# Optimization experiments

Measured on AMD Instinct MI355X. Metric: run time of the kernel, lower is better.

Reference implementation:

```python
import jax, jax.numpy as jnp
import numpy as np

N, E = 25000, 400000
HID, EDGE_F, DIM, HEADS, ADY = 128, 16, 3, 8, 64
INNER = int(1.25 * HID)          # 160
MSG_F = 2 * HID + EDGE_F + 1     # 273 (e3, relaxed=False -> 1 distance feature)


def silu(x):
    return x * jax.nn.sigmoid(x)


def ada_ln(x, y, W, b):
    # LayerNorm (no affine) + FiLM conditioning from y
    mu = jnp.mean(x, axis=-1, keepdims=True)
    var = jnp.var(x, axis=-1, keepdims=True)
    xn = (x - mu) * jax.lax.rsqrt(var + 1e-5)
    scale, shift = jnp.split(y @ W + b, 2, axis=-1)
    return xn * (1.0 + scale) + shift


def setup_inputs() -> dict:
    key = jax.random.key(0)
    ks = jax.random.split(key, 32)
    rn = lambda k, shp, s=0.05: (jax.random.normal(k, shp, jnp.float32) * s)
    inp = {
        'h': jax.random.normal(ks[0], (N, HID), jnp.float32),
        'coords': jax.random.normal(ks[1], (N, DIM), jnp.float32),
        'a': jax.random.normal(ks[2], (E, EDGE_F), jnp.float32),
        'y': jax.random.normal(ks[3], (N, ADY), jnp.float32),
        'res': jnp.zeros((N, HID), jnp.float32),
        'src': jax.random.randint(ks[4], (E,), 0, N, jnp.int32),
        'dst': jax.random.randint(ks[5], (E,), 0, N, jnp.int32),
        # edge MLP
        'We1': rn(ks[6], (MSG_F, INNER)), 'be1': jnp.zeros((INNER,), jnp.float32),
        'We2': rn(ks[7], (INNER, INNER)), 'be2': jnp.zeros((INNER,), jnp.float32),
        # coord head (xavier gain 0.001 -> tiny init)
        'Wc': rn(ks[8], (INNER, 1), 0.001),
        # attention/value/output heads
        'Wv': rn(ks[9], (INNER, HID)),
        'Wa': rn(ks[10], (INNER, HEADS)),
        'Wo': rn(ks[11], (HID, HID)),
        # node MLP
        'Wn1': rn(ks[12], (HID, INNER)), 'bn1': jnp.zeros((INNER,), jnp.float32),
        'Wn2': rn(ks[13], (INNER, HID)), 'bn2': jnp.zeros((HID,), jnp.float32),
        # adaptive LayerNorms (FiLM from y)
        'Wf1': rn(ks[14], (ADY, 2 * HID)), 'bf1': jnp.zeros((2 * HID,), jnp.float32),
        'Wf2': rn(ks[15], (ADY, 2 * HID)), 'bf2': jnp.zeros((2 * HID,), jnp.float32),
    }
    return inp


def reference(h, coords, a, y, res, src, dst,
              We1, be1, We2, be2, Wc, Wv, Wa, Wo,
              Wn1, bn1, Wn2, bn2, Wf1, bf1, Wf2, bf2):
    n = h.shape[0]
    heads = Wa.shape[1]
    # --- distance features (e3, relaxed=False): radial only ---
    xs, xd = coords[src], coords[dst]          # [E, 3]
    diffs = xs - xd
    radials = jnp.sum(diffs * diffs, axis=-1, keepdims=True)  # [E, 1]
    # --- edge MLP on gathered features ---
    f = jnp.concatenate([h[src], h[dst], radials, a], axis=-1)  # [E, 273]
    m = silu(f @ We1 + be1)
    m = silu(m @ We2 + be2)                    # [E, inner]
    # --- coordinate messages + scatter-sum to dst ---
    msg_x = (m @ Wc) * diffs / (jnp.sqrt(radials + 1e-5) + 1.0)  # [E, 3]
    coords_out = coords + jax.ops.segment_sum(msg_x, dst, num_segments=n)
    # --- edge softmax over incoming edges per dst node ---
    logits = m @ Wa                             # [E, heads]
    mx = jax.ops.segment_max(logits, dst, num_segments=n)
    ex = jnp.exp(logits - mx[dst])
    den = jax.ops.segment_sum(ex, dst, num_segments=n)
    w = ex / den[dst]                           # [E, heads]
    # --- weighted value aggregation ---
    vals = (m @ Wv).reshape(-1, heads, HID // heads) * w[:, :, None]
    h_agg = jax.ops.segment_sum(vals, dst, num_segments=n).reshape(n, HID)
    f2 = h_agg @ Wo
    res1 = res + f2
    h1 = ada_ln(h + f2, y, Wf1, bf1)
    f3 = silu(h1 @ Wn1 + bn1) @ Wn2 + bn2
    res2 = res1 + f3
    h2 = ada_ln(h1 + f3, y, Wf2, bf2)
    return (h2, coords_out, res2)
```

## Files before the change

kernel.cpp:

```cpp
#include <hip/hip_runtime.h>
#include <math.h>

#define N_NODES 25000
#define N_EDGES 400000
#define HID 128
#define EDGE_F 16
#define ADY 64
#define INNER 160
#define MSG_F 273
#define HEADS 8

#define OUT_CRD (N_NODES * HID)
#define OUT_RES (N_NODES * (HID + 3))

#define FLAG_OFF 0
#define DEN_OFF  256
#define CACC_OFF 800256
#define HAGG_OFF 1100288
#define CW_BASE  13900288
#define MEMSET_BYTES 13900288

typedef unsigned short u16;
typedef unsigned int u32;
typedef unsigned long long u64;
typedef __attribute__((ext_vector_type(8))) short short8;
typedef __attribute__((ext_vector_type(4))) float f32x4;

__device__ __forceinline__ float bf2f(u16 v) {
    union { u32 u; float f; } x; x.u = ((u32)v) << 16; return x.f;
}
__device__ __forceinline__ u16 f2bf(float f) {
    union { float ff; u32 u; } x; x.ff = f;
    u32 u = x.u;
    u32 rounding = 0x7FFFu + ((u >> 16) & 1u);
    u += rounding;
    return (u16)(u >> 16);
}
__device__ __forceinline__ float silu(float z) {
    z = fminf(fmaxf(z, -30000.f), 30000.f);
    return z / (1.0f + __expf(-z));
}

template<bool F32> __device__ __forceinline__ float ldg1(const void* p, size_t i) {
    if (F32) return ((const float*)p)[i];
    return bf2f(((const u16*)p)[i]);
}
template<bool F32> __device__ __forceinline__ void stg1(void* p, size_t i, float v) {
    if (F32) ((float*)p)[i] = v;
    else     ((u16*)p)[i] = f2bf(v);
}
template<bool F32> __device__ __forceinline__ void ld8a(const void* p, size_t i, u16* dst) {
    if (F32) {
        const float* fp = (const float*)p + i;
        float4 v0 = ((const float4*)fp)[0];
        float4 v1 = ((const float4*)fp)[1];
        __align__(16) u16 tmp[8] = { f2bf(v0.x), f2bf(v0.y), f2bf(v0.z), f2bf(v0.w),
                                     f2bf(v1.x), f2bf(v1.y), f2bf(v1.z), f2bf(v1.w) };
        *(uint4*)dst = *(const uint4*)tmp;
    } else {
        *(uint4*)dst = *(const uint4*)((const u16*)p + i);
    }
}
__device__ __forceinline__ float ldany(const void* p, size_t i, bool f32) {
    return f32 ? ((const float*)p)[i] : bf2f(((const u16*)p)[i]);
}

__global__ void detect_kernel(const void* h, int* flag) {
    __shared__ float red[256];
    const int t = threadIdx.x;
    const u16* p = (const u16*)h;
    float mx = 0.f;
    for (int i = 0; i < 8; i++) {
        int idx = (t * 8 + i) * 97;
        float v = fabsf(bf2f(p[idx * 2]));
        mx = fmaxf(mx, v);
    }
    red[t] = mx;
    __syncthreads();
    for (int s = 128; s > 0; s >>= 1) {
        if (t < s) red[t] = fmaxf(red[t], red[t + s]);
        __syncthreads();
    }
    if (t == 0) flag[0] = (red[0] > 1e10f || red[0] == 0.f) ? 1 : 0;
}

struct CvtArgs {
    const void* src[16];
    u64 dstoff[16];
    int n[16];
};
__global__ void cvt_kernel(const int* __restrict__ flag, char* wsbase, CvtArgs args) {
    const int ten = blockIdx.y;
    const void* s = args.src[ten];
    u16* d = (u16*)(wsbase + args.dstoff[ten]);
    const int n = args.n[ten];
    const bool f32 = (*flag != 0);
    if (f32) {
        const float* sf = (const float*)s;
        for (int i = blockIdx.x * 256 + threadIdx.x; i < n; i += gridDim.x * 256)
            d[i] = f2bf(sf[i]);
    } else {
        const u16* su = (const u16*)s;
        for (int i = blockIdx.x * 256 + threadIdx.x; i < n; i += gridDim.x * 256)
            d[i] = su[i];
    }
}

__global__ void blockw_kernel(const int* __restrict__ flag, char* ws,
                              u64 b1off, u64 b2off, u64 b3off, u64 b4off,
                              u64 b5off, u64 b6off, u64 b7off, u64 b8off,
                              const void* We1, const void* We2,
                              const void* Wv, const void* Wa, const void* Wc,
                              const void* Wo, const void* Wn1, const void* Wn2,
                              const void* Wf1, const void* Wf2)
{
    const bool f32 = (*flag != 0);
    u16* b1 = (u16*)(ws + b1off);
    u16* b2 = (u16*)(ws + b2off);
    u16* b3 = (u16*)(ws + b3off);
    u16* b4 = (u16*)(ws + b4off);
    u16* b5 = (u16*)(ws + b5off);
    u16* b6 = (u16*)(ws + b6off);
    u16* b7 = (u16*)(ws + b7off);
    u16* b8 = (u16*)(ws + b8off);
    const int g = blockIdx.x * 256 + threadIdx.x;
    const int stride = gridDim.x * 256;
    for (int i = g; i < 5*160*72; i += stride) {
        int c = i / (160*72), rem = i % (160*72), n = rem / 72, kc = rem % 72;
        int k = c*64 + kc;
        float v = 0.f;
        if (kc < 64) {
            if (k < MSG_F)      v = ldany(We1, (size_t)k*INNER + n, f32);
            else if (k == 273)  v = ldany(We1, (size_t)256*INNER + n, f32);
        }
        b1[i] = f2bf(v);
    }
    for (int i = g; i < 3*160*72; i += stride) {
        int c = i / (160*72), rem = i % (160*72), n = rem / 72, kc = rem % 72;
        int k = c*64 + kc;
        float v = 0.f;
        if (kc < 64 && k < INNER) v = ldany(We2, (size_t)k*INNER + n, f32);
        b2[i] = f2bf(v);
    }
    for (int i = g; i < 3*144*72; i += stride) {
        int c = i / (144*72), rem = i % (144*72), n = rem / 72, kc = rem % 72;
        int k = c*64 + kc;
        float v = 0.f;
        if (kc < 64 && k < INNER) {
            if (n < 128)      v = ldany(Wv, (size_t)k*HID + n, f32);
            else if (n < 136) v = ldany(Wa, (size_t)k*HEADS + (n-128), f32);
            else if (n == 136) v = ldany(Wc, (size_t)k, f32);
        }
        b3[i] = f2bf(v);
    }
    for (int i = g; i < 2*128*72; i += stride) {
        int c = i / (128*72), rem = i % (128*72), n = rem / 72, kc = rem % 72;
        int k = c*64 + kc;
        float v = (kc < 64 && k < HID) ? ldany(Wo, (size_t)k*HID + n, f32) : 0.f;
        b4[i] = f2bf(v);
    }
    for (int i = g; i < 2*160*72; i += stride) {
        int c = i / (160*72), rem = i % (160*72), n = rem / 72, kc = rem % 72;
        int k = c*64 + kc;
        float v = (kc < 64) ? ldany(Wn1, (size_t)k*INNER + n, f32) : 0.f;
        b5[i] = f2bf(v);
    }
    for (int i = g; i < 3*128*72; i += stride) {
        int c = i / (128*72), rem = i % (128*72), n = rem / 72, kc = rem % 72;
        int k = c*64 + kc;
        float v = (kc < 64 && k < INNER) ? ldany(Wn2, (size_t)k*HID + n, f32) : 0.f;
        b6[i] = f2bf(v);
    }
    for (int i = g; i < 256*72; i += stride) {
        int n = i / 72, kc = i % 72;
        float v = (kc < 64) ? ldany(Wf1, (size_t)kc*256 + n, f32) : 0.f;
        b7[i] = f2bf(v);
    }
    for (int i = g; i < 256*72; i += stride) {
        int n = i / 72, kc = i % 72;
        float v = (kc < 64) ? ldany(Wf2, (size_t)kc*256 + n, f32) : 0.f;
        b8[i] = f2bf(v);
    }
}

template<bool F32>
__device__ __forceinline__ void edge_body(
    const void* h, const void* coords, const void* a,
    const int* __restrict__ src, const int* __restrict__ dst,
    const u16* __restrict__ We1Tb, const u16* __restrict__ We2Tb,
    const u16* __restrict__ W3Tb,
    const u16* __restrict__ cbe1, const u16* __restrict__ cbe2,
    float* __restrict__ den, float* __restrict__ hagg, float* __restrict__ cacc,
    u16* sPool, float* sex, float* sdiff, float* srad, int* ssrc, int* sdstl)
{
    const int t   = threadIdx.x;
    const int w   = t >> 6;
    const int l   = t & 63;
    const int col = l & 15;
    const int q   = l >> 4;

    u16* sF  = sPool;
    u16* sM1 = sPool;
    u16* sM2 = sPool + 64*168;

    const int e0 = blockIdx.x * 64;

    if (t < 64) {
        int e = e0 + t;
        int s = src[e], d = dst[e];
        ssrc[t] = s; sdstl[t] = d;
        float dx = ldg1<F32>(coords, (size_t)s*3+0) - ldg1<F32>(coords, (size_t)d*3+0);
        float dy = ldg1<F32>(coords, (size_t)s*3+1) - ldg1<F32>(coords, (size_t)d*3+1);
        float dz = ldg1<F32>(coords, (size_t)s*3+2) - ldg1<F32>(coords, (size_t)d*3+2);
        sdiff[t*4+0] = dx; sdiff[t*4+1] = dy; sdiff[t*4+2] = dz;
        float r2 = dx*dx + dy*dy + dz*dz;
        srad[t] = r2;
        sdiff[t*4+3] = 1.0f / (sqrtf(r2 + 1e-5f) + 1.0f);
    }
    __syncthreads();

    {
        int e = t >> 2, part = t & 3;
        int node_s = ssrc[e], node_d = sdstl[e];
        #pragma unroll
        for (int c = 0; c < 4; c++) {
            int node = (c < 2) ? node_s : node_d;
            int c0 = (c & 1) * 64 + part * 16;
            ld8a<F32>(h, (size_t)node*HID + c0,     &sF[e*360 + c*72 + part*16]);
            ld8a<F32>(h, (size_t)node*HID + c0 + 8, &sF[e*360 + c*72 + part*16 + 8]);
        }
        __align__(16) u16 tmp[16];
        #pragma unroll
        for (int j = 0; j < 16; j++) tmp[j] = 0;
        if (part == 0) {
            float r2 = srad[e];
            tmp[0] = f2bf(r2);
            for (int j = 0; j < 15; j++)
                tmp[1+j] = f2bf(ldg1<F32>(a, (size_t)(e0+e)*EDGE_F + j));
        } else if (part == 1) {
            tmp[0] = f2bf(ldg1<F32>(a, (size_t)(e0+e)*EDGE_F + 15));
            float r2 = srad[e];
            tmp[1] = f2bf(r2 - bf2f(f2bf(r2)));
        }
        *(uint4*)(&sF[e*360 + 4*72 + part*16])     = ((uint4*)tmp)[0];
        *(uint4*)(&sF[e*360 + 4*72 + part*16 + 8]) = ((uint4*)tmp)[1];
    }
    __syncthreads();

    f32x4 acc1[10];
    #pragma unroll
    for (int nt = 0; nt < 10; nt++) {
        float v = bf2f(cbe1[nt*16 + col]);
        acc1[nt] = (f32x4){v, v, v, v};
    }
    const u16* fbase = &sF[(w*16 + col)*360];
    #pragma unroll
    for (int c = 0; c < 5; c++) {
        #pragma unroll
        for (int ks = 0; ks < 2; ks++) {
            short8 af = *(const short8*)(fbase + c*72 + ks*32 + q*8);
            const u16* B1 = We1Tb + (size_t)c*160*72 + ks*32 + q*8;
            #pragma unroll
            for (int nt = 0; nt < 10; nt++) {
                short8 b = *(const short8*)(B1 + (nt*16 + col)*72);
                acc1[nt] = __builtin_amdgcn_mfma_f32_16x16x32_bf16(af, b, acc1[nt], 0, 0, 0);
            }
        }
    }
    __syncthreads();
    #pragma unroll
    for (int nt = 0; nt < 10; nt++)
        #pragma unroll
        for (int r = 0; r < 4; r++)
            sM1[(w*16 + q*4 + r)*168 + nt*16 + col] = f2bf(silu(acc1[nt][r]));
    __syncthreads();

    f32x4 acc2[10];
    #pragma unroll
    for (int nt = 0; nt < 10; nt++) {
        float v = bf2f(cbe2[nt*16 + col]);
        acc2[nt] = (f32x4){v, v, v, v};
    }
    const u16* m1base = &sM1[(w*16 + col)*168];
    #pragma unroll
    for (int k5 = 0; k5 < 5; k5++) {
        short8 af = *(const short8*)(m1base + k5*32 + q*8);
        const u16* B2 = We2Tb + (size_t)(k5>>1)*160*72 + (k5&1)*32 + q*8;
        #pragma unroll
        for (int nt = 0; nt < 10; nt++) {
            short8 b = *(const short8*)(B2 + (nt*16 + col)*72);
            acc2[nt] = __builtin_amdgcn_mfma_f32_16x16x32_bf16(af, b, acc2[nt], 0, 0, 0);
        }
    }
    #pragma unroll
    for (int nt = 0; nt < 10; nt++)
        #pragma unroll
        for (int r = 0; r < 4; r++)
            sM2[(w*16 + q*4 + r)*168 + nt*16 + col] = f2bf(silu(acc2[nt][r]));
    __syncthreads();

    f32x4 acc3[9];
    #pragma unroll
    for (int nt = 0; nt < 9; nt++) acc3[nt] = (f32x4){0.f, 0.f, 0.f, 0.f};
    const u16* m2base = &sM2[(w*16 + col)*168];
    #pragma unroll
    for (int k5 = 0; k5 < 5; k5++) {
        short8 af = *(const short8*)(m2base + k5*32 + q*8);
        const u16* B3 = W3Tb + (size_t)(k5>>1)*144*72 + (k5&1)*32 + q*8;
        #pragma unroll
        for (int nt = 0; nt < 9; nt++) {
            short8 b = *(const short8*)(B3 + (nt*16 + col)*72);
            acc3[nt] = __builtin_amdgcn_mfma_f32_16x16x32_bf16(af, b, acc3[nt], 0, 0, 0);
        }
    }

    const int mbase = w*16 + q*4;
    if (col < 8) {
        #pragma unroll
        for (int r = 0; r < 4; r++) {
            int m = mbase + r;
            int d = sdstl[m];
            float ex = __expf(fminf(fmaxf(acc3[8][r], -30.f), 30.f));
            sex[m*8 + col] = ex;
            atomicAdd(&den[(size_t)d*8 + col], ex);
        }
    } else if (col == 8) {
        #pragma unroll
        for (int r = 0; r < 4; r++) {
            int m = mbase + r;
            int d = sdstl[m];
            float lc = fminf(fmaxf(acc3[8][r], -1e6f), 1e6f);
            float invf = sdiff[m*4 + 3];
            #pragma unroll
            for (int j = 0; j < 3; j++)
                atomicAdd(&cacc[(size_t)d*3 + j], lc * sdiff[m*4 + j] * invf);
        }
    }
    __syncthreads();
    #pragma unroll
    for (int nt = 0; nt < 8; nt++) {
        #pragma unroll
        for (int r = 0; r < 4; r++) {
            int m = mbase + r;
            int d = sdstl[m];
            atomicAdd(&hagg[(size_t)d*HID + nt*16 + col], acc3[nt][r] * sex[m*8 + nt]);
        }
    }
}

__global__ __launch_bounds__(256, 3)
void edge_kernel(const int* __restrict__ flag,
                 const void* h, const void* coords, const void* a,
                 const int* __restrict__ src, const int* __restrict__ dst,
                 const u16* __restrict__ We1Tb, const u16* __restrict__ We2Tb,
                 const u16* __restrict__ W3Tb,
                 const u16* __restrict__ cbe1, const u16* __restrict__ cbe2,
                 float* __restrict__ den, float* __restrict__ hagg,
                 float* __restrict__ cacc)
{
    __shared__ __align__(16) u16 sPool[64*360];
    __shared__ float sex[64*8];
    __shared__ float sdiff[64*4];
    __shared__ float srad[64];
    __shared__ int   ssrc[64];
    __shared__ int   sdstl[64];
    if (*flag)
        edge_body<true>(h, coords, a, src, dst, We1Tb, We2Tb, W3Tb, cbe1, cbe2,
                        den, hagg, cacc, sPool, sex, sdiff, srad, ssrc, sdstl);
    else
        edge_body<false>(h, coords, a, src, dst, We1Tb, We2Tb, W3Tb, cbe1, cbe2,
                         den, hagg, cacc, sPool, sex, sdiff, srad, ssrc, sdstl);
}

template<bool F32>
__device__ __forceinline__ void node_body(
    const void* h, const void* res, const void* coords, const void* y,
    const float* __restrict__ den, const float* __restrict__ hagg,
    const float* __restrict__ cacc,
    const u16* __restrict__ WoB, const u16* __restrict__ Wn1B,
    const u16* __restrict__ Wn2B, const u16* __restrict__ Wf1B,
    const u16* __restrict__ Wf2B,
    const u16* __restrict__ cbn1, const u16* __restrict__ cbn2,
    const u16* __restrict__ cbf1, const u16* __restrict__ cbf2,
    void* out,
    u16* sB, u16* sG, u16* sM, u16* sM2, u16* sR1, u16* sH, u16* sY)
{
    const int t = threadIdx.x;
    const int w = t >> 6, l = t & 63, col = l & 15, q = l >> 4;
    const int n0 = blockIdx.x * 64;

    {
        int node = t >> 2, part = t & 3;
        int gn = n0 + node;
        bool ok = gn < N_NODES;
        uint4 z = {0,0,0,0};
        #pragma unroll
        for (int j = 0; j < 32; j += 8) {
            if (ok) ld8a<F32>(h, (size_t)gn*HID + part*32 + j, &sH[node*136 + part*32 + j]);
            else    *(uint4*)&sH[node*136 + part*32 + j] = z;
        }
        if (ok) {
            ld8a<F32>(y, (size_t)gn*ADY + part*16,     &sY[node*72 + part*16]);
            ld8a<F32>(y, (size_t)gn*ADY + part*16 + 8, &sY[node*72 + part*16 + 8]);
        } else {
            *(uint4*)&sY[node*72 + part*16]     = z;
            *(uint4*)&sY[node*72 + part*16 + 8] = z;
        }
        #pragma unroll
        for (int c = 0; c < 2; c++) {
            float inv = 0.f;
            if (ok) {
                float dd = den[(size_t)gn*8 + c*4 + part];
                inv = dd > 0.f ? 1.f/dd : 0.f;
            }
            __align__(16) u16 tmp[16];
            #pragma unroll
            for (int j = 0; j < 16; j += 4) {
                float4 v = ok ? *(const float4*)(hagg + (size_t)gn*HID + c*64 + part*16 + j)
                              : (float4){0.f,0.f,0.f,0.f};
                tmp[j+0]=f2bf(v.x*inv); tmp[j+1]=f2bf(v.y*inv);
                tmp[j+2]=f2bf(v.z*inv); tmp[j+3]=f2bf(v.w*inv);
            }
            *(uint4*)&sG[c*4608 + node*72 + part*16]     = ((uint4*)tmp)[0];
            *(uint4*)&sG[c*4608 + node*72 + part*16 + 8] = ((uint4*)tmp)[1];
        }
    }

    f32x4 aF2[8];
    #pragma unroll
    for (int nt = 0; nt < 8; nt++) aF2[nt] = (f32x4){0.f,0.f,0.f,0.f};
    for (int c = 0; c < 2; c++) {
        __syncthreads();
        { const uint4* g4 = (const uint4*)(WoB + (size_t)c*128*72); uint4* s4 = (uint4*)sB;
          for (int i = t; i < 1152; i += 256) s4[i] = g4[i]; }
        __syncthreads();
        #pragma unroll
        for (int ks = 0; ks < 2; ks++) {
            short8 af = *(const short8*)&sG[c*4608 + (w*16+col)*72 + ks*32 + q*8];
            #pragma unroll
            for (int nt = 0; nt < 8; nt++) {
                short8 b = *(const short8*)&sB[(nt*16+col)*72 + ks*32 + q*8];
                aF2[nt] = __builtin_amdgcn_mfma_f32_16x16x32_bf16(af, b, aF2[nt], 0, 0, 0);
            }
        }
    }

    f32x4 aFl[16];
    #pragma unroll
    for (int nt = 0; nt < 16; nt++) {
        float v = bf2f(cbf1[nt*16 + col]);
        aFl[nt] = (f32x4){v,v,v,v};
    }
    __syncthreads();
    { const uint4* g4 = (const uint4*)Wf1B; uint4* s4 = (uint4*)sB;
      for (int i = t; i < 2304; i += 256) s4[i] = g4[i]; }
    __syncthreads();
    #pragma unroll
    for (int ks = 0; ks < 2; ks++) {
        short8 af = *(const short8*)&sY[(w*16+col)*72 + ks*32 + q*8];
        #pragma unroll
        for (int nt = 0; nt < 16; nt++) {
            short8 b = *(const short8*)&sB[(nt*16+col)*72 + ks*32 + q*8];
            aFl[nt] = __builtin_amdgcn_mfma_f32_16x16x32_bf16(af, b, aFl[nt], 0, 0, 0);
        }
    }

    {
        float xv[8][4], s[4], ss[4];
        #pragma unroll
        for (int r = 0; r < 4; r++) { s[r] = 0.f; ss[r] = 0.f; }
        #pragma unroll
        for (int nt = 0; nt < 8; nt++)
            #pragma unroll
            for (int r = 0; r < 4; r++) {
                float x = bf2f(sH[(w*16+q*4+r)*136 + nt*16+col]) + aF2[nt][r];
                xv[nt][r] = x; s[r] += x; ss[r] += x*x;
            }
        #pragma unroll
        for (int r = 0; r < 4; r++)
            for (int off = 1; off <= 8; off <<= 1) {
                s[r]  += __shfl_xor(s[r], off);
                ss[r] += __shfl_xor(ss[r], off);
            }
        float mu[4], rs[4];
        #pragma unroll
        for (int r = 0; r < 4; r++) {
            mu[r] = s[r] * (1.f/128.f);
            float var = ss[r] * (1.f/128.f) - mu[r]*mu[r];
            rs[r] = rsqrtf(fmaxf(var, 0.f) + 1e-5f);
        }
        #pragma unroll
        for (int nt = 0; nt < 8; nt++)
            #pragma unroll
            for (int r = 0; r < 4; r++) {
                int m = w*16+q*4+r, n = nt*16+col, gn = n0+m;
                float h1 = (xv[nt][r]-mu[r])*rs[r]*(1.f+aFl[nt][r]) + aFl[nt+8][r];
                sM[m*168 + n] = f2bf(h1);
                float r1 = aF2[nt][r];
                if (gn < N_NODES) r1 += ldg1<F32>(res, (size_t)gn*HID + n);
                sR1[m*128 + n] = f2bf(r1);
            }
    }

    f32x4 aT[10];
    #pragma unroll
    for (int nt = 0; nt < 10; nt++) {
        float v = bf2f(cbn1[nt*16 + col]);
        aT[nt] = (f32x4){v,v,v,v};
    }
    for (int c = 0; c < 2; c++) {
        __syncthreads();
        { const uint4* g4 = (const uint4*)(Wn1B + (size_t)c*160*72); uint4* s4 = (uint4*)sB;
          for (int i = t; i < 1440; i += 256) s4[i] = g4[i]; }
        __syncthreads();
        #pragma unroll
        for (int ks = 0; ks < 2; ks++) {
            short8 af = *(const short8*)&sM[(w*16+col)*168 + c*64 + ks*32 + q*8];
            #pragma unroll
            for (int nt = 0; nt < 10; nt++) {
                short8 b = *(const short8*)&sB[(nt*16+col)*72 + ks*32 + q*8];
                aT[nt] = __builtin_amdgcn_mfma_f32_16x16x32_bf16(af, b, aT[nt], 0, 0, 0);
            }
        }
    }
    #pragma unroll
    for (int nt = 0; nt < 10; nt++)
        #pragma unroll
        for (int r = 0; r < 4; r++)
            sM2[(w*16+q*4+r)*168 + nt*16+col] = f2bf(silu(aT[nt][r]));

    f32x4 aF3[8];
    #pragma unroll
    for (int nt = 0; nt < 8; nt++) {
        float v = bf2f(cbn2[nt*16 + col]);
        aF3[nt] = (f32x4){v,v,v,v};
    }
    for (int c = 0; c < 3; c++) {
        __syncthreads();
        { const uint4* g4 = (const uint4*)(Wn2B + (size_t)c*128*72); uint4* s4 = (uint4*)sB;
          for (int i = t; i < 1152; i += 256) s4[i] = g4[i]; }
        __syncthreads();
        const int nks = (c < 2) ? 2 : 1;
        for (int ks = 0; ks < nks; ks++) {
            short8 af = *(const short8*)&sM2[(w*16+col)*168 + c*64 + ks*32 + q*8];
            #pragma unroll
            for (int nt = 0; nt < 8; nt++) {
                short8 b = *(const short8*)&sB[(nt*16+col)*72 + ks*32 + q*8];
                aF3[nt] = __builtin_amdgcn_mfma_f32_16x16x32_bf16(af, b, aF3[nt], 0, 0, 0);
            }
        }
    }

    #pragma unroll
    for (int nt = 0; nt < 16; nt++) {
        float v = bf2f(cbf2[nt*16 + col]);
        aFl[nt] = (f32x4){v,v,v,v};
    }
    __syncthreads();
    { const uint4* g4 = (const uint4*)Wf2B; uint4* s4 = (uint4*)sB;
      for (int i = t; i < 2304; i += 256) s4[i] = g4[i]; }
    __syncthreads();
    #pragma unroll
    for (int ks = 0; ks < 2; ks++) {
        short8 af = *(const short8*)&sY[(w*16+col)*72 + ks*32 + q*8];
        #pragma unroll
        for (int nt = 0; nt < 16; nt++) {
            short8 b = *(const short8*)&sB[(nt*16+col)*72 + ks*32 + q*8];
            aFl[nt] = __builtin_amdgcn_mfma_f32_16x16x32_bf16(af, b, aFl[nt], 0, 0, 0);
        }
    }

    {
        float xv[8][4], s[4], ss[4];
        #pragma unroll
        for (int r = 0; r < 4; r++) { s[r] = 0.f; ss[r] = 0.f; }
        #pragma unroll
        for (int nt = 0; nt < 8; nt++)
            #pragma unroll
            for (int r = 0; r < 4; r++) {
                float x = bf2f(sM[(w*16+q*4+r)*168 + nt*16+col]) + aF3[nt][r];
                xv[nt][r] = x; s[r] += x; ss[r] += x*x;
            }
        #pragma unroll
        for (int r = 0; r < 4; r++)
            for (int off = 1; off <= 8; off <<= 1) {
                s[r]  += __shfl_xor(s[r], off);
                ss[r] += __shfl_xor(ss[r], off);
            }
        float mu[4], rs[4];
        #pragma unroll
        for (int r = 0; r < 4; r++) {
            mu[r] = s[r] * (1.f/128.f);
            float var = ss[r] * (1.f/128.f) - mu[r]*mu[r];
            rs[r] = rsqrtf(fmaxf(var, 0.f) + 1e-5f);
        }
        #pragma unroll
        for (int nt = 0; nt < 8; nt++)
            #pragma unroll
            for (int r = 0; r < 4; r++) {
                int m = w*16+q*4+r, n = nt*16+col, gn = n0+m;
                if (gn < N_NODES) {
                    float h2 = (xv[nt][r]-mu[r])*rs[r]*(1.f+aFl[nt][r]) + aFl[nt+8][r];
                    stg1<F32>(out, (size_t)gn*HID + n, h2);
                    stg1<F32>(out, (size_t)OUT_RES + (size_t)gn*HID + n,
                              bf2f(sR1[m*128 + n]) + aF3[nt][r]);
                }
            }
    }

    if (t < 64) {
        int gn = n0 + t;
        if (gn < N_NODES) {
            #pragma unroll
            for (int j = 0; j < 3; j++)
                stg1<F32>(out, (size_t)OUT_CRD + (size_t)gn*3 + j,
                          ldg1<F32>(coords, (size_t)gn*3 + j) + cacc[(size_t)gn*3 + j]);
        }
    }
}

__global__ __launch_bounds__(256, 1)
void node_kernel(const int* __restrict__ flag,
                 const void* h, const void* res, const void* coords, const void* y,
                 const float* __restrict__ den, const float* __restrict__ hagg,
                 const float* __restrict__ cacc,
                 const u16* __restrict__ WoB, const u16* __restrict__ Wn1B,
                 const u16* __restrict__ Wn2B, const u16* __restrict__ Wf1B,
                 const u16* __restrict__ Wf2B,
                 const u16* __restrict__ cbn1, const u16* __restrict__ cbn2,
                 const u16* __restrict__ cbf1, const u16* __restrict__ cbf2,
                 void* out)
{
    __shared__ __align__(16) u16 sB[256*72];
    __shared__ __align__(16) u16 sG[2*64*72];
    __shared__ __align__(16) u16 sM[64*168];
    __shared__ __align__(16) u16 sM2[64*168];
    __shared__ __align__(16) u16 sR1[64*128];
    __shared__ __align__(16) u16 sH[64*136];
    __shared__ __align__(16) u16 sY[64*72];
    if (*flag)
        node_body<true>(h, res, coords, y, den, hagg, cacc, WoB, Wn1B, Wn2B,
                        Wf1B, Wf2B, cbn1, cbn2, cbf1, cbf2, out,
                        sB, sG, sM, sM2, sR1, sH, sY);
    else
        node_body<false>(h, res, coords, y, den, hagg, cacc, WoB, Wn1B, Wn2B,
                         Wf1B, Wf2B, cbn1, cbn2, cbf1, cbf2, out,
                         sB, sG, sM, sM2, sR1, sH, sY);
}

extern "C" void kernel_launch(void* const* d_in, const int* in_sizes, int n_in,
                              void* d_out, int out_size, void* d_ws, size_t ws_size,
                              hipStream_t stream)
{
    const void* h      = d_in[0];
    const void* coords = d_in[1];
    const void* a      = d_in[2];
    const void* y      = d_in[3];
    const void* res    = d_in[4];
    const int* src     = (const int*)d_in[5];
    const int* dst     = (const int*)d_in[6];

    char* ws = (char*)d_ws;
    int*   flag = (int*)(ws + FLAG_OFF);
    float* den  = (float*)(ws + DEN_OFF);
    float* cacc = (float*)(ws + CACC_OFF);
    float* hagg = (float*)(ws + HAGG_OFF);

    const int wn[16]  = {43680, 25600, 20480, 1280, 160, 160, 160, 16384,
                         20480, 160, 20480, 128, 16384, 256, 16384, 256};
    const int widx[16] = {7, 9, 12, 13, 11, 8, 10, 14, 15, 16, 17, 18, 19, 20, 21, 22};
    u64 off = CW_BASE;
    CvtArgs args;
    u64 offs[16];
    for (int i = 0; i < 16; i++) {
        args.src[i] = d_in[widx[i]];
        args.dstoff[i] = off;
        args.n[i] = wn[i];
        offs[i] = off;
        off += (u64)wn[i] * 2;
    }
    u64 bw1 = (off + 255) & ~(u64)255;
    u64 bw2 = bw1 + (u64)5*160*72*2;
    u64 bw3 = bw2 + (u64)3*160*72*2;
    u64 bw4 = bw3 + (u64)3*144*72*2;
    u64 bw5 = bw4 + (u64)2*128*72*2;
    u64 bw6 = bw5 + (u64)2*160*72*2;
    u64 bw7 = bw6 + (u64)3*128*72*2;
    u64 bw8 = bw7 + (u64)256*72*2;

    const u16* cbe1 = (const u16*)(ws + offs[5]);
    const u16* cbe2 = (const u16*)(ws + offs[6]);
    const u16* cbn1 = (const u16*)(ws + offs[9]);
    const u16* cbn2 = (const u16*)(ws + offs[11]);
    const u16* cbf1 = (const u16*)(ws + offs[13]);
    const u16* cbf2 = (const u16*)(ws + offs[15]);
    const u16* We1Tb = (const u16*)(ws + bw1);
    const u16* We2Tb = (const u16*)(ws + bw2);
    const u16* W3Tb  = (const u16*)(ws + bw3);
    const u16* WoB   = (const u16*)(ws + bw4);
    const u16* Wn1B  = (const u16*)(ws + bw5);
    const u16* Wn2B  = (const u16*)(ws + bw6);
    const u16* Wf1B  = (const u16*)(ws + bw7);
    const u16* Wf2B  = (const u16*)(ws + bw8);

    hipMemsetAsync(d_ws, 0, MEMSET_BYTES, stream);

    detect_kernel<<<1, 256, 0, stream>>>(h, flag);
    cvt_kernel<<<dim3(8, 16), 256, 0, stream>>>(flag, ws, args);
    blockw_kernel<<<64, 256, 0, stream>>>(flag, ws, bw1, bw2, bw3, bw4,
                                          bw5, bw6, bw7, bw8,
                                          d_in[7], d_in[9], d_in[12], d_in[13], d_in[11],
                                          d_in[14], d_in[15], d_in[17], d_in[19], d_in[21]);

    edge_kernel<<<N_EDGES/64, 256, 0, stream>>>(flag, h, coords, a, src, dst,
                                                We1Tb, We2Tb, W3Tb, cbe1, cbe2,
                                                den, hagg, cacc);

    node_kernel<<<(N_NODES + 63)/64, 256, 0, stream>>>(
        flag, h, res, coords, y, den, hagg, cacc,
        WoB, Wn1B, Wn2B, Wf1B, Wf2B, cbn1, cbn2, cbf1, cbf2, d_out);
}
```

Before: 574.6 us.

## Make edge and node kernels wave-independent, loading MFMA fragments directly from global memory

Both the edge and node kernels now let each wave own its 16 rows end to end. MFMA A-fragments are gathered directly from global memory into registers instead of being staged through block-shared tiles, and weight B-fragments are read from global/L2 instead of cooperative LDS copies. Block-wide __syncthreads are replaced by per-wave LDS fences, shared memory shrinks to a small per-wave scratch, and launch bounds are raised so more blocks fit per CU. The cost is more global/L2 traffic for weights and gathers, recomputed coordinate diffs, and higher register pressure from keeping h1/res1 in registers.

```diff
diff --git a/kernel.cpp b/kernel.cpp
--- a/kernel.cpp
+++ b/kernel.cpp
@@ -49,20 +49,25 @@
     if (F32) ((float*)p)[i] = v;
     else     ((u16*)p)[i] = f2bf(v);
 }
-template<bool F32> __device__ __forceinline__ void ld8a(const void* p, size_t i, u16* dst) {
+template<bool F32> __device__ __forceinline__ short8 ldfragA(const void* p, size_t i) {
     if (F32) {
-        const float* fp = (const float*)p + i;
-        float4 v0 = ((const float4*)fp)[0];
-        float4 v1 = ((const float4*)fp)[1];
-        __align__(16) u16 tmp[8] = { f2bf(v0.x), f2bf(v0.y), f2bf(v0.z), f2bf(v0.w),
-                                     f2bf(v1.x), f2bf(v1.y), f2bf(v1.z), f2bf(v1.w) };
-        *(uint4*)dst = *(const uint4*)tmp;
+        const float4* fp = (const float4*)((const float*)p + i);
+        float4 v0 = fp[0], v1 = fp[1];
+        union { u16 s[8]; short8 v; } u;
+        u.s[0]=f2bf(v0.x); u.s[1]=f2bf(v0.y); u.s[2]=f2bf(v0.z); u.s[3]=f2bf(v0.w);
+        u.s[4]=f2bf(v1.x); u.s[5]=f2bf(v1.y); u.s[6]=f2bf(v1.z); u.s[7]=f2bf(v1.w);
+        return u.v;
     } else {
-        *(uint4*)dst = *(const uint4*)((const u16*)p + i);
+        return *(const short8*)((const u16*)p + i);
     }
 }
 __device__ __forceinline__ float ldany(const void* p, size_t i, bool f32) {
     return f32 ? ((const float*)p)[i] : bf2f(((const u16*)p)[i]);
+}
+__device__ __forceinline__ void wave_lds_fence() {
+    __builtin_amdgcn_wave_barrier();
+    __builtin_amdgcn_s_waitcnt(0xc07f);
+    __builtin_amdgcn_wave_barrier();
 }
 
 __global__ void detect_kernel(const void* h, int* flag) {
@@ -191,61 +196,30 @@
     const u16* __restrict__ W3Tb,
     const u16* __restrict__ cbe1, const u16* __restrict__ cbe2,
     float* __restrict__ den, float* __restrict__ hagg, float* __restrict__ cacc,
-    u16* sPool, float* sex, float* sdiff, float* srad, int* ssrc, int* sdstl)
+    u16* sScr)
 {
     const int t   = threadIdx.x;
     const int w   = t >> 6;
     const int l   = t & 63;
     const int col = l & 15;
     const int q   = l >> 4;
-
-    u16* sF  = sPool;
-    u16* sM1 = sPool;
-    u16* sM2 = sPool + 64*168;
-
-    const int e0 = blockIdx.x * 64;
-
-    if (t < 64) {
-        int e = e0 + t;
-        int s = src[e], d = dst[e];
-        ssrc[t] = s; sdstl[t] = d;
-        float dx = ldg1<F32>(coords, (size_t)s*3+0) - ldg1<F32>(coords, (size_t)d*3+0);
-        float dy = ldg1<F32>(coords, (size_t)s*3+1) - ldg1<F32>(coords, (size_t)d*3+1);
-        float dz = ldg1<F32>(coords, (size_t)s*3+2) - ldg1<F32>(coords, (size_t)d*3+2);
-        sdiff[t*4+0] = dx; sdiff[t*4+1] = dy; sdiff[t*4+2] = dz;
-        float r2 = dx*dx + dy*dy + dz*dz;
-        srad[t] = r2;
-        sdiff[t*4+3] = 1.0f / (sqrtf(r2 + 1e-5f) + 1.0f);
-    }
-    __syncthreads();
-
+    const int ebase = blockIdx.x * 64 + w * 16;
+
+    u16* sc = sScr + w * 16 * 168;
+
+    const int myedge = ebase + col;
+    const int s_col = src[myedge];
+    const int d_col = dst[myedge];
+    float r2col;
     {
-        int e = t >> 2, part = t & 3;
-        int node_s = ssrc[e], node_d = sdstl[e];
-        #pragma unroll
-        for (int c = 0; c < 4; c++) {
-            int node = (c < 2) ? node_s : node_d;
-            int c0 = (c & 1) * 64 + part * 16;
-            ld8a<F32>(h, (size_t)node*HID + c0,     &sF[e*360 + c*72 + part*16]);
-            ld8a<F32>(h, (size_t)node*HID + c0 + 8, &sF[e*360 + c*72 + part*16 + 8]);
-        }
-        __align__(16) u16 tmp[16];
-        #pragma unroll
-        for (int j = 0; j < 16; j++) tmp[j] = 0;
-        if (part == 0) {
-            float r2 = srad[e];
-            tmp[0] = f2bf(r2);
-            for (int j = 0; j < 15; j++)
-                tmp[1+j] = f2bf(ldg1<F32>(a, (size_t)(e0+e)*EDGE_F + j));
-        } else if (part == 1) {
-            tmp[0] = f2bf(ldg1<F32>(a, (size_t)(e0+e)*EDGE_F + 15));
-            float r2 = srad[e];
-            tmp[1] = f2bf(r2 - bf2f(f2bf(r2)));
-        }
-        *(uint4*)(&sF[e*360 + 4*72 + part*16])     = ((uint4*)tmp)[0];
-        *(uint4*)(&sF[e*360 + 4*72 + part*16 + 8]) = ((uint4*)tmp)[1];
-    }
-    __syncthreads();
+        float dx = ldg1<F32>(coords, (size_t)s_col*3+0) - ldg1<F32>(coords, (size_t)d_col*3+0);
+        float dy = ldg1<F32>(coords, (size_t)s_col*3+1) - ldg1<F32>(coords, (size_t)d_col*3+1);
+        float dz = ldg1<F32>(coords, (size_t)s_col*3+2) - ldg1<F32>(coords, (size_t)d_col*3+2);
+        r2col = dx*dx + dy*dy + dz*dz;
+    }
+    int dstep[4];
+    #pragma unroll
+    for (int r = 0; r < 4; r++) dstep[r] = dst[ebase + q*4 + r];
 
     f32x4 acc1[10];
     #pragma unroll
@@ -253,12 +227,12 @@
         float v = bf2f(cbe1[nt*16 + col]);
         acc1[nt] = (f32x4){v, v, v, v};
     }
-    const u16* fbase = &sF[(w*16 + col)*360];
-    #pragma unroll
-    for (int c = 0; c < 5; c++) {
+    #pragma unroll
+    for (int c = 0; c < 4; c++) {
+        const int node = (c < 2) ? s_col : d_col;
         #pragma unroll
         for (int ks = 0; ks < 2; ks++) {
-            short8 af = *(const short8*)(fbase + c*72 + ks*32 + q*8);
+            short8 af = ldfragA<F32>(h, (size_t)node*HID + (c&1)*64 + ks*32 + q*8);
             const u16* B1 = We1Tb + (size_t)c*160*72 + ks*32 + q*8;
             #pragma unroll
             for (int nt = 0; nt < 10; nt++) {
@@ -267,13 +241,34 @@
             }
         }
     }
-    __syncthreads();
+    {
+        float r2hi = bf2f(f2bf(r2col));
+        float r2lo = r2col - r2hi;
+        #pragma unroll
+        for (int ks = 0; ks < 2; ks++) {
+            union { u16 s[8]; short8 v; } u;
+            #pragma unroll
+            for (int j = 0; j < 8; j++) {
+                int f = ks*32 + q*8 + j;
+                float av = (f >= 1 && f <= 16)
+                         ? ldg1<F32>(a, (size_t)myedge*EDGE_F + (f-1)) : 0.f;
+                float fv = (f == 0) ? r2col : (f == 17) ? r2lo : av;
+                u.s[j] = f2bf(fv);
+            }
+            const u16* B1 = We1Tb + (size_t)4*160*72 + ks*32 + q*8;
+            #pragma unroll
+            for (int nt = 0; nt < 10; nt++) {
+                short8 b = *(const short8*)(B1 + (nt*16 + col)*72);
+                acc1[nt] = __builtin_amdgcn_mfma_f32_16x16x32_bf16(u.v, b, acc1[nt], 0, 0, 0);
+            }
+        }
+    }
     #pragma unroll
     for (int nt = 0; nt < 10; nt++)
         #pragma unroll
         for (int r = 0; r < 4; r++)
-            sM1[(w*16 + q*4 + r)*168 + nt*16 + col] = f2bf(silu(acc1[nt][r]));
-    __syncthreads();
+            sc[(q*4 + r)*168 + nt*16 + col] = f2bf(silu(acc1[nt][r]));
+    wave_lds_fence();
 
     f32x4 acc2[10];
     #pragma unroll
@@ -281,10 +276,9 @@
         float v = bf2f(cbe2[nt*16 + col]);
         acc2[nt] = (f32x4){v, v, v, v};
     }
-    const u16* m1base = &sM1[(w*16 + col)*168];
     #pragma unroll
     for (int k5 = 0; k5 < 5; k5++) {
-        short8 af = *(const short8*)(m1base + k5*32 + q*8);
+        short8 af = *(const short8*)(sc + col*168 + k5*32 + q*8);
         const u16* B2 = We2Tb + (size_t)(k5>>1)*160*72 + (k5&1)*32 + q*8;
         #pragma unroll
         for (int nt = 0; nt < 10; nt++) {
@@ -296,16 +290,15 @@
     for (int nt = 0; nt < 10; nt++)
         #pragma unroll
         for (int r = 0; r < 4; r++)
-            sM2[(w*16 + q*4 + r)*168 + nt*16 + col] = f2bf(silu(acc2[nt][r]));
-    __syncthreads();
+            sc[(q*4 + r)*168 + nt*16 + col] = f2bf(silu(acc2[nt][r]));
+    wave_lds_fence();
 
     f32x4 acc3[9];
     #pragma unroll
     for (int nt = 0; nt < 9; nt++) acc3[nt] = (f32x4){0.f, 0.f, 0.f, 0.f};
-    const u16* m2base = &sM2[(w*16 + col)*168];
     #pragma unroll
     for (int k5 = 0; k5 < 5; k5++) {
-        short8 af = *(const short8*)(m2base + k5*32 + q*8);
+        short8 af = *(const short8*)(sc + col*168 + k5*32 + q*8);
         const u16* B3 = W3Tb + (size_t)(k5>>1)*144*72 + (k5&1)*32 + q*8;
         #pragma unroll
         for (int nt = 0; nt < 9; nt++) {
@@ -314,41 +307,44 @@
         }
     }
 
-    const int mbase = w*16 + q*4;
+    float exv[4] = {0.f, 0.f, 0.f, 0.f};
     if (col < 8) {
         #pragma unroll
         for (int r = 0; r < 4; r++) {
-            int m = mbase + r;
-            int d = sdstl[m];
             float ex = __expf(fminf(fmaxf(acc3[8][r], -30.f), 30.f));
-            sex[m*8 + col] = ex;
-            atomicAdd(&den[(size_t)d*8 + col], ex);
+            exv[r] = ex;
+            atomicAdd(&den[(size_t)dstep[r]*8 + col], ex);
         }
     } else if (col == 8) {
         #pragma unroll
         for (int r = 0; r < 4; r++) {
-            int m = mbase + r;
-            int d = sdstl[m];
-            float lc = fminf(fmaxf(acc3[8][r], -1e6f), 1e6f);
-            float invf = sdiff[m*4 + 3];
-            #pragma unroll
-            for (int j = 0; j < 3; j++)
-                atomicAdd(&cacc[(size_t)d*3 + j], lc * sdiff[m*4 + j] * invf);
-        }
-    }
-    __syncthreads();
+            int e = ebase + q*4 + r;
+            int ss = src[e], dd = dstep[r];
+            float dx = ldg1<F32>(coords, (size_t)ss*3+0) - ldg1<F32>(coords, (size_t)dd*3+0);
+            float dy = ldg1<F32>(coords, (size_t)ss*3+1) - ldg1<F32>(coords, (size_t)dd*3+1);
+            float dz = ldg1<F32>(coords, (size_t)ss*3+2) - ldg1<F32>(coords, (size_t)dd*3+2);
+            float r2 = dx*dx + dy*dy + dz*dz;
+            float invf = 1.0f / (sqrtf(r2 + 1e-5f) + 1.0f);
+            float lc = fminf(fmaxf(acc3[8][r], -1e6f), 1e6f) * invf;
+            atomicAdd(&cacc[(size_t)dd*3 + 0], lc * dx);
+            atomicAdd(&cacc[(size_t)dd*3 + 1], lc * dy);
+            atomicAdd(&cacc[(size_t)dd*3 + 2], lc * dz);
+        }
+    }
     #pragma unroll
     for (int nt = 0; nt < 8; nt++) {
-        #pragma unroll
-        for (int r = 0; r < 4; r++) {
-            int m = mbase + r;
-            int d = sdstl[m];
-            atomicAdd(&hagg[(size_t)d*HID + nt*16 + col], acc3[nt][r] * sex[m*8 + nt]);
-        }
-    }
-}
-
-__global__ __launch_bounds__(256, 3)
+        float e0 = __shfl(exv[0], q*16 + nt);
+        float e1 = __shfl(exv[1], q*16 + nt);
+        float e2 = __shfl(exv[2], q*16 + nt);
+        float e3 = __shfl(exv[3], q*16 + nt);
+        atomicAdd(&hagg[(size_t)dstep[0]*HID + nt*16 + col], acc3[nt][0] * e0);
+        atomicAdd(&hagg[(size_t)dstep[1]*HID + nt*16 + col], acc3[nt][1] * e1);
+        atomicAdd(&hagg[(size_t)dstep[2]*HID + nt*16 + col], acc3[nt][2] * e2);
+        atomicAdd(&hagg[(size_t)dstep[3]*HID + nt*16 + col], acc3[nt][3] * e3);
+    }
+}
+
+__global__ __launch_bounds__(256, 4)
 void edge_kernel(const int* __restrict__ flag,
                  const void* h, const void* coords, const void* a,
                  const int* __restrict__ src, const int* __restrict__ dst,
@@ -358,18 +354,13 @@
                  float* __restrict__ den, float* __restrict__ hagg,
                  float* __restrict__ cacc)
 {
-    __shared__ __align__(16) u16 sPool[64*360];
-    __shared__ float sex[64*8];
-    __shared__ float sdiff[64*4];
-    __shared__ float srad[64];
-    __shared__ int   ssrc[64];
-    __shared__ int   sdstl[64];
+    __shared__ __align__(16) u16 sScr[4 * 16 * 168];
     if (*flag)
         edge_body<true>(h, coords, a, src, dst, We1Tb, We2Tb, W3Tb, cbe1, cbe2,
-                        den, hagg, cacc, sPool, sex, sdiff, srad, ssrc, sdstl);
+                        den, hagg, cacc, sScr);
     else
         edge_body<false>(h, coords, a, src, dst, We1Tb, We2Tb, W3Tb, cbe1, cbe2,
-                         den, hagg, cacc, sPool, sex, sdiff, srad, ssrc, sdstl);
+                         den, hagg, cacc, sScr);
 }
 
 template<bool F32>
@@ -382,65 +373,44 @@
     const u16* __restrict__ Wf2B,
     const u16* __restrict__ cbn1, const u16* __restrict__ cbn2,
     const u16* __restrict__ cbf1, const u16* __restrict__ cbf2,
-    void* out,
-    u16* sB, u16* sG, u16* sM, u16* sM2, u16* sR1, u16* sH, u16* sY)
+    void* out, u16* sScr)
 {
     const int t = threadIdx.x;
     const int w = t >> 6, l = t & 63, col = l & 15, q = l >> 4;
-    const int n0 = blockIdx.x * 64;
-
-    {
-        int node = t >> 2, part = t & 3;
-        int gn = n0 + node;
-        bool ok = gn < N_NODES;
-        uint4 z = {0,0,0,0};
-        #pragma unroll
-        for (int j = 0; j < 32; j += 8) {
-            if (ok) ld8a<F32>(h, (size_t)gn*HID + part*32 + j, &sH[node*136 + part*32 + j]);
-            else    *(uint4*)&sH[node*136 + part*32 + j] = z;
-        }
-        if (ok) {
-            ld8a<F32>(y, (size_t)gn*ADY + part*16,     &sY[node*72 + part*16]);
-            ld8a<F32>(y, (size_t)gn*ADY + part*16 + 8, &sY[node*72 + part*16 + 8]);
-        } else {
-            *(uint4*)&sY[node*72 + part*16]     = z;
-            *(uint4*)&sY[node*72 + part*16 + 8] = z;
-        }
-        #pragma unroll
-        for (int c = 0; c < 2; c++) {
-            float inv = 0.f;
-            if (ok) {
-                float dd = den[(size_t)gn*8 + c*4 + part];
-                inv = dd > 0.f ? 1.f/dd : 0.f;
-            }
-            __align__(16) u16 tmp[16];
-            #pragma unroll
-            for (int j = 0; j < 16; j += 4) {
-                float4 v = ok ? *(const float4*)(hagg + (size_t)gn*HID + c*64 + part*16 + j)
-                              : (float4){0.f,0.f,0.f,0.f};
-                tmp[j+0]=f2bf(v.x*inv); tmp[j+1]=f2bf(v.y*inv);
-                tmp[j+2]=f2bf(v.z*inv); tmp[j+3]=f2bf(v.w*inv);
-            }
-            *(uint4*)&sG[c*4608 + node*72 + part*16]     = ((uint4*)tmp)[0];
-            *(uint4*)&sG[c*4608 + node*72 + part*16 + 8] = ((uint4*)tmp)[1];
-        }
-    }
+    const int nodew = blockIdx.x * 64 + w * 16;
+    const int mynode = nodew + col;
+    const bool okA = mynode < N_NODES;
+    u16* sc = sScr + w * 16 * 168;
+
+    int gm[4]; bool okC[4];
+    #pragma unroll
+    for (int r = 0; r < 4; r++) { gm[r] = nodew + q*4 + r; okC[r] = gm[r] < N_NODES; }
 
     f32x4 aF2[8];
     #pragma unroll
     for (int nt = 0; nt < 8; nt++) aF2[nt] = (f32x4){0.f,0.f,0.f,0.f};
+    #pragma unroll
     for (int c = 0; c < 2; c++) {
-        __syncthreads();
-        { const uint4* g4 = (const uint4*)(WoB + (size_t)c*128*72); uint4* s4 = (uint4*)sB;
-          for (int i = t; i < 1152; i += 256) s4[i] = g4[i]; }
-        __syncthreads();
         #pragma unroll
         for (int ks = 0; ks < 2; ks++) {
-            short8 af = *(const short8*)&sG[c*4608 + (w*16+col)*72 + ks*32 + q*8];
+            const int kbase = c*64 + ks*32 + q*8;
+            union { u16 s[8]; short8 v; } u;
+            if (okA) {
+                float dd = den[(size_t)mynode*8 + (kbase >> 4)];
+                float inv = dd > 0.f ? 1.f/dd : 0.f;
+                const float4* gp = (const float4*)(hagg + (size_t)mynode*HID + kbase);
+                float4 v0 = gp[0], v1 = gp[1];
+                u.s[0]=f2bf(v0.x*inv); u.s[1]=f2bf(v0.y*inv); u.s[2]=f2bf(v0.z*inv); u.s[3]=f2bf(v0.w*inv);
+                u.s[4]=f2bf(v1.x*inv); u.s[5]=f2bf(v1.y*inv); u.s[6]=f2bf(v1.z*inv); u.s[7]=f2bf(v1.w*inv);
+            } else {
+                #pragma unroll
+                for (int j = 0; j < 8; j++) u.s[j] = 0;
+            }
+            const u16* B = WoB + (size_t)c*128*72 + ks*32 + q*8;
             #pragma unroll
             for (int nt = 0; nt < 8; nt++) {
-                short8 b = *(const short8*)&sB[(nt*16+col)*72 + ks*32 + q*8];
-                aF2[nt] = __builtin_amdgcn_mfma_f32_16x16x32_bf16(af, b, aF2[nt], 0, 0, 0);
+                short8 b = *(const short8*)(B + (nt*16 + col)*72);
+                aF2[nt] = __builtin_amdgcn_mfma_f32_16x16x32_bf16(u.v, b, aF2[nt], 0, 0, 0);
             }
         }
     }
@@ -451,20 +421,20 @@
         float v = bf2f(cbf1[nt*16 + col]);
         aFl[nt] = (f32x4){v,v,v,v};
     }
-    __syncthreads();
-    { const uint4* g4 = (const uint4*)Wf1B; uint4* s4 = (uint4*)sB;
-      for (int i = t; i < 2304; i += 256) s4[i] = g4[i]; }
-    __syncthreads();
     #pragma unroll
     for (int ks = 0; ks < 2; ks++) {
-        short8 af = *(const short8*)&sY[(w*16+col)*72 + ks*32 + q*8];
+        short8 af;
+        if (okA) af = ldfragA<F32>(y, (size_t)mynode*ADY + ks*32 + q*8);
+        else { union { u16 s[8]; short8 v; } z; for (int j=0;j<8;j++) z.s[j]=0; af = z.v; }
+        const u16* B = Wf1B + ks*32 + q*8;
         #pragma unroll
         for (int nt = 0; nt < 16; nt++) {
-            short8 b = *(const short8*)&sB[(nt*16+col)*72 + ks*32 + q*8];
+            short8 b = *(const short8*)(B + (nt*16 + col)*72);
             aFl[nt] = __builtin_amdgcn_mfma_f32_16x16x32_bf16(af, b, aFl[nt], 0, 0, 0);
         }
     }
 
+    float h1c[8][4], r1c[8][4];
     {
         float xv[8][4], s[4], ss[4];
         #pragma unroll
@@ -473,7 +443,8 @@
         for (int nt = 0; nt < 8; nt++)
             #pragma unroll
             for (int r = 0; r < 4; r++) {
-                float x = bf2f(sH[(w*16+q*4+r)*136 + nt*16+col]) + aF2[nt][r];
+                float hv = okC[r] ? ldg1<F32>(h, (size_t)gm[r]*HID + nt*16 + col) : 0.f;
+                float x = hv + aF2[nt][r];
                 xv[nt][r] = x; s[r] += x; ss[r] += x*x;
             }
         #pragma unroll
@@ -482,25 +453,22 @@
                 s[r]  += __shfl_xor(s[r], off);
                 ss[r] += __shfl_xor(ss[r], off);
             }
-        float mu[4], rs[4];
         #pragma unroll
         for (int r = 0; r < 4; r++) {
-            mu[r] = s[r] * (1.f/128.f);
-            float var = ss[r] * (1.f/128.f) - mu[r]*mu[r];
-            rs[r] = rsqrtf(fmaxf(var, 0.f) + 1e-5f);
-        }
-        #pragma unroll
-        for (int nt = 0; nt < 8; nt++)
-            #pragma unroll
-            for (int r = 0; r < 4; r++) {
-                int m = w*16+q*4+r, n = nt*16+col, gn = n0+m;
-                float h1 = (xv[nt][r]-mu[r])*rs[r]*(1.f+aFl[nt][r]) + aFl[nt+8][r];
-                sM[m*168 + n] = f2bf(h1);
-                float r1 = aF2[nt][r];
-                if (gn < N_NODES) r1 += ldg1<F32>(res, (size_t)gn*HID + n);
-                sR1[m*128 + n] = f2bf(r1);
-            }
-    }
+            float mu = s[r] * (1.f/128.f);
+            float var = ss[r] * (1.f/128.f) - mu*mu;
+            float rs = rsqrtf(fmaxf(var, 0.f) + 1e-5f);
+            #pragma unroll
+            for (int nt = 0; nt < 8; nt++) {
+                float h1 = (xv[nt][r]-mu)*rs*(1.f+aFl[nt][r]) + aFl[nt+8][r];
+                h1c[nt][r] = h1;
+                float rv = okC[r] ? ldg1<F32>(res, (size_t)gm[r]*HID + nt*16 + col) : 0.f;
+                r1c[nt][r] = rv + aF2[nt][r];
+                sc[(q*4 + r)*168 + nt*16 + col] = f2bf(h1);
+            }
+        }
+    }
+    wave_lds_fence();
 
     f32x4 aT[10];
     #pragma unroll
@@ -508,17 +476,15 @@
         float v = bf2f(cbn1[nt*16 + col]);
         aT[nt] = (f32x4){v,v,v,v};
     }
+    #pragma unroll
     for (int c = 0; c < 2; c++) {
-        __syncthreads();
-        { const uint4* g4 = (const uint4*)(Wn1B + (size_t)c*160*72); uint4* s4 = (uint4*)sB;
-          for (int i = t; i < 1440; i += 256) s4[i] = g4[i]; }
-        __syncthreads();
         #pragma unroll
         for (int ks = 0; ks < 2; ks++) {
-            short8 af = *(const short8*)&sM[(w*16+col)*168 + c*64 + ks*32 + q*8];
+            short8 af = *(const short8*)(sc + col*168 + c*64 + ks*32 + q*8);
+            const u16* B = Wn1B + (size_t)c*160*72 + ks*32 + q*8;
             #pragma unroll
             for (int nt = 0; nt < 10; nt++) {
-                short8 b = *(const short8*)&sB[(nt*16+col)*72 + ks*32 + q*8];
+                short8 b = *(const short8*)(B + (nt*16 + col)*72);
                 aT[nt] = __builtin_amdgcn_mfma_f32_16x16x32_bf16(af, b, aT[nt], 0, 0, 0);
             }
         }
@@ -527,7 +493,8 @@
     for (int nt = 0; nt < 10; nt++)
         #pragma unroll
         for (int r = 0; r < 4; r++)
-            sM2[(w*16+q*4+r)*168 + nt*16+col] = f2bf(silu(aT[nt][r]));
+            sc[(q*4 + r)*168 + nt*16 + col] = f2bf(silu(aT[nt][r]));
+    wave_lds_fence();
 
     f32x4 aF3[8];
     #pragma unroll
@@ -535,19 +502,14 @@
         float v = bf2f(cbn2[nt*16 + col]);
         aF3[nt] = (f32x4){v,v,v,v};
     }
-    for (int c = 0; c < 3; c++) {
-        __syncthreads();
-        { const uint4* g4 = (const uint4*)(Wn2B + (size_t)c*128*72); uint4* s4 = (uint4*)sB;
-          for (int i = t; i < 1152; i += 256) s4[i] = g4[i]; }
-        __syncthreads();
-        const int nks = (c < 2) ? 2 : 1;
-        for (int ks = 0; ks < nks; ks++) {
-            short8 af = *(const short8*)&sM2[(w*16+col)*168 + c*64 + ks*32 + q*8];
-            #pragma unroll
-            for (int nt = 0; nt < 8; nt++) {
-                short8 b = *(const short8*)&sB[(nt*16+col)*72 + ks*32 + q*8];
-                aF3[nt] = __builtin_amdgcn_mfma_f32_16x16x32_bf16(af, b, aF3[nt], 0, 0, 0);
-            }
+    #pragma unroll
+    for (int k5 = 0; k5 < 5; k5++) {
+        short8 af = *(const short8*)(sc + col*168 + k5*32 + q*8);
+        const u16* B = Wn2B + (size_t)(k5>>1)*128*72 + (k5&1)*32 + q*8;
+        #pragma unroll
+        for (int nt = 0; nt < 8; nt++) {
+            short8 b = *(const short8*)(B + (nt*16 + col)*72);
+            aF3[nt] = __builtin_amdgcn_mfma_f32_16x16x32_bf16(af, b, aF3[nt], 0, 0, 0);
         }
     }
 
@@ -556,16 +518,15 @@
         float v = bf2f(cbf2[nt*16 + col]);
         aFl[nt] = (f32x4){v,v,v,v};
     }
-    __syncthreads();
-    { const uint4* g4 = (const uint4*)Wf2B; uint4* s4 = (uint4*)sB;
-      for (int i = t; i < 2304; i += 256) s4[i] = g4[i]; }
-    __syncthreads();
     #pragma unroll
     for (int ks = 0; ks < 2; ks++) {
-        short8 af = *(const short8*)&sY[(w*16+col)*72 + ks*32 + q*8];
+        short8 af;
+        if (okA) af = ldfragA<F32>(y, (size_t)mynode*ADY + ks*32 + q*8);
+        else { union { u16 s[8]; short8 v; } z; for (int j=0;j<8;j++) z.s[j]=0; af = z.v; }
+        const u16* B = Wf2B + ks*32 + q*8;
         #pragma unroll
         for (int nt = 0; nt < 16; nt++) {
-            short8 b = *(const short8*)&sB[(nt*16+col)*72 + ks*32 + q*8];
+            short8 b = *(const short8*)(B + (nt*16 + col)*72);
             aFl[nt] = __builtin_amdgcn_mfma_f32_16x16x32_bf16(af, b, aFl[nt], 0, 0, 0);
         }
     }
@@ -578,7 +539,7 @@
         for (int nt = 0; nt < 8; nt++)
             #pragma unroll
             for (int r = 0; r < 4; r++) {
-                float x = bf2f(sM[(w*16+q*4+r)*168 + nt*16+col]) + aF3[nt][r];
+                float x = h1c[nt][r] + aF3[nt][r];
                 xv[nt][r] = x; s[r] += x; ss[r] += x*x;
             }
         #pragma unroll
@@ -587,39 +548,33 @@
                 s[r]  += __shfl_xor(s[r], off);
                 ss[r] += __shfl_xor(ss[r], off);
             }
-        float mu[4], rs[4];
         #pragma unroll
         for (int r = 0; r < 4; r++) {
-            mu[r] = s[r] * (1.f/128.f);
-            float var = ss[r] * (1.f/128.f) - mu[r]*mu[r];
-            rs[r] = rsqrtf(fmaxf(var, 0.f) + 1e-5f);
-        }
-        #pragma unroll
-        for (int nt = 0; nt < 8; nt++)
-            #pragma unroll
-            for (int r = 0; r < 4; r++) {
-                int m = w*16+q*4+r, n = nt*16+col, gn = n0+m;
-                if (gn < N_NODES) {
-                    float h2 = (xv[nt][r]-mu[r])*rs[r]*(1.f+aFl[nt][r]) + aFl[nt+8][r];
-                    stg1<F32>(out, (size_t)gn*HID + n, h2);
-                    stg1<F32>(out, (size_t)OUT_RES + (size_t)gn*HID + n,
-                              bf2f(sR1[m*128 + n]) + aF3[nt][r]);
+            float mu = s[r] * (1.f/128.f);
+            float var = ss[r] * (1.f/128.f) - mu*mu;
+            float rs = rsqrtf(fmaxf(var, 0.f) + 1e-5f);
+            if (okC[r]) {
+                #pragma unroll
+                for (int nt = 0; nt < 8; nt++) {
+                    int n = nt*16 + col;
+                    float h2 = (xv[nt][r]-mu)*rs*(1.f+aFl[nt][r]) + aFl[nt+8][r];
+                    stg1<F32>(out, (size_t)gm[r]*HID + n, h2);
+                    stg1<F32>(out, (size_t)OUT_RES + (size_t)gm[r]*HID + n,
+                              r1c[nt][r] + aF3[nt][r]);
                 }
             }
-    }
-
-    if (t < 64) {
-        int gn = n0 + t;
-        if (gn < N_NODES) {
-            #pragma unroll
-            for (int j = 0; j < 3; j++)
-                stg1<F32>(out, (size_t)OUT_CRD + (size_t)gn*3 + j,
-                          ldg1<F32>(coords, (size_t)gn*3 + j) + cacc[(size_t)gn*3 + j]);
-        }
-    }
-}
-
-__global__ __launch_bounds__(256, 1)
+        }
+    }
+
+    if (q == 0 && okA) {
+        #pragma unroll
+        for (int j = 0; j < 3; j++)
+            stg1<F32>(out, (size_t)OUT_CRD + (size_t)mynode*3 + j,
+                      ldg1<F32>(coords, (size_t)mynode*3 + j) + cacc[(size_t)mynode*3 + j]);
+    }
+}
+
+__global__ __launch_bounds__(256, 2)
 void node_kernel(const int* __restrict__ flag,
                  const void* h, const void* res, const void* coords, const void* y,
                  const float* __restrict__ den, const float* __restrict__ hagg,
@@ -631,21 +586,13 @@
                  const u16* __restrict__ cbf1, const u16* __restrict__ cbf2,
                  void* out)
 {
-    __shared__ __align__(16) u16 sB[256*72];
-    __shared__ __align__(16) u16 sG[2*64*72];
-    __shared__ __align__(16) u16 sM[64*168];
-    __shared__ __align__(16) u16 sM2[64*168];
-    __shared__ __align__(16) u16 sR1[64*128];
-    __shared__ __align__(16) u16 sH[64*136];
-    __shared__ __align__(16) u16 sY[64*72];
+    __shared__ __align__(16) u16 sScr[4 * 16 * 168];
     if (*flag)
         node_body<true>(h, res, coords, y, den, hagg, cacc, WoB, Wn1B, Wn2B,
-                        Wf1B, Wf2B, cbn1, cbn2, cbf1, cbf2, out,
-                        sB, sG, sM, sM2, sR1, sH, sY);
+                        Wf1B, Wf2B, cbn1, cbn2, cbf1, cbf2, out, sScr);
     else
         node_body<false>(h, res, coords, y, den, hagg, cacc, WoB, Wn1B, Wn2B,
-                         Wf1B, Wf2B, cbn1, cbn2, cbf1, cbf2, out,
-                         sB, sG, sM, sM2, sR1, sH, sY);
+                         Wf1B, Wf2B, cbn1, cbn2, cbf1, cbf2, out, sScr);
 }
 
 extern "C" void kernel_launch(void* const* d_in, const int* in_sizes, int n_in,
```

Measured after the change: 647.4 us. 1.13x slower.
